# Kernel optimization log

Measured on AMD Instinct MI355X. Metric: run time of the kernel, lower is better.

## Reference

```python
import jax, jax.numpy as jnp
import numpy as np

N_NODES = 50000
N_EDGES = 600000
IN_CH = 128
HID_CH = 256
OUT_CH = 128


def setup_inputs() -> dict:
    key = jax.random.key(0)
    ks = jax.random.split(key, 8)
    x = jax.random.normal(ks[0], (N_NODES, IN_CH), dtype=jnp.float32)
    edge_index = jax.random.randint(ks[1], (2, N_EDGES), 0, N_NODES, dtype=jnp.int32)
    # SAGEConv params: lin_l applied to aggregated neighbors, lin_r to root, bias on lin_l
    def init_w(k, fan_in, fan_out):
        bound = 1.0 / np.sqrt(fan_in)
        return jax.random.uniform(k, (fan_in, fan_out), jnp.float32, -bound, bound)
    W_l1 = init_w(ks[2], IN_CH, HID_CH)
    W_r1 = init_w(ks[3], IN_CH, HID_CH)
    b1 = jnp.zeros((HID_CH,), jnp.float32)
    W_l2 = init_w(ks[4], HID_CH, OUT_CH)
    W_r2 = init_w(ks[5], HID_CH, OUT_CH)
    b2 = jnp.zeros((OUT_CH,), jnp.float32)
    return {"x": x, "edge_index": edge_index, "W_l1": W_l1, "W_r1": W_r1,
            "b1": b1, "W_l2": W_l2, "W_r2": W_r2, "b2": b2}


def _sage_conv(x, src, dst, W_l, W_r, b):
    # mean-aggregate neighbor messages: gather from src, scatter-sum to dst
    msg = x[src]                                        # [E, d]
    agg = jax.ops.segment_sum(msg, dst, num_segments=N_NODES)      # [N, d]
    cnt = jax.ops.segment_sum(jnp.ones_like(dst, dtype=x.dtype), dst,
                              num_segments=N_NODES)                 # [N]
    mean = agg / jnp.maximum(cnt, 1.0)[:, None]
    return mean @ W_l + x @ W_r + b


def reference(x, edge_index, W_l1, W_r1, b1, W_l2, W_r2, b2):
    src, dst = edge_index[0], edge_index[1]
    h = _sage_conv(x, src, dst, W_l1, W_r1, b1)
    h = jax.nn.relu(h)
    # Dropout(0.3) is identity in eval mode
    out = _sage_conv(h, src, dst, W_l2, W_r2, b2)
    return out
```

## Files before the change

kernel.cpp:

```cpp
#include <hip/hip_runtime.h>


typedef __attribute__((ext_vector_type(8))) short short8;
typedef __attribute__((ext_vector_type(4))) short short4v;
typedef __attribute__((ext_vector_type(4))) float f32x4;

constexpr int ELL = 48;

__device__ inline unsigned short f2b(float f) {
    union { float f; unsigned int u; } v; v.f = f;
    unsigned int u = v.u + 0x7FFFu + ((v.u >> 16) & 1u);
    return (unsigned short)(u >> 16);
}
__device__ inline float b2f(unsigned short h) {
    union { unsigned int u; float f; } v; v.u = ((unsigned int)h) << 16;
    return v.f;
}

__global__ __launch_bounds__(256) void prep_k(
    const float* __restrict__ x,
    const float* __restrict__ Wl1, const float* __restrict__ Wr1,
    const float* __restrict__ Wl2, const float* __restrict__ Wr2,
    unsigned short* __restrict__ x_bf,
    unsigned short* __restrict__ Wt1, unsigned short* __restrict__ Wt2,
    int* __restrict__ cnt,
    long n4, int N, int nbF2b, int nbW)
{
    int b = blockIdx.x;
    const int tid = threadIdx.x;
    if (b < nbF2b) {
        long i = (long)b * 256 + tid;
        if (i < n4) {
            float4 v = *(const float4*)(x + i * 4);
            short4v o;
            o[0] = (short)f2b(v.x); o[1] = (short)f2b(v.y);
            o[2] = (short)f2b(v.z); o[3] = (short)f2b(v.w);
            *(short4v*)(x_bf + i * 4) = o;
        }
        return;
    }
    b -= nbF2b;
    if (b < nbW) {
        int y = b >> 7;
        int idx = (b & 127) * 256 + tid;
        const float* src = (y == 0) ? Wl1 : (y == 1) ? Wr1 : (y == 2) ? Wl2 : Wr2;
        unsigned short* dst = (y < 2) ? (Wt1 + (size_t)y * 32768)
                                      : (Wt2 + (size_t)(y - 2) * 32768);
        int K1 = (y < 2) ? 128 : 256;
        int H  = (y < 2) ? 256 : 128;
        int n = idx / K1, k = idx % K1;
        dst[idx] = f2b(src[(size_t)k * H + n]);
        return;
    }
    b -= nbW;
    int i = b * 256 + tid;
    if (i < N / 4) ((int4*)cnt)[i] = (int4){0, 0, 0, 0};
}

__global__ __launch_bounds__(256) void fill_ell_k(
    const int* __restrict__ src, const int* __restrict__ dst,
    int* __restrict__ cnt, unsigned short* __restrict__ nbr, int E)
{
    int e = blockIdx.x * blockDim.x + threadIdx.x;
    if (e >= E) return;
    int d = dst[e];
    int p = atomicAdd(&cnt[d], 1);
    if (p < ELL) nbr[(size_t)d * ELL + p] = (unsigned short)src[e];
}

template<int C>
__device__ inline void ell_row_sum(
    const unsigned short* __restrict__ feat,
    const unsigned short* __restrict__ row,
    int deg, int g, float (&acc)[8])
{
    int i = 0;
    for (; i + 4 <= deg; i += 4) {
        ushort4 s4 = *(const ushort4*)(row + i);
        short8 v0 = *(const short8*)(feat + (size_t)s4.x * C + g * 8);
        short8 v1 = *(const short8*)(feat + (size_t)s4.y * C + g * 8);
        short8 v2 = *(const short8*)(feat + (size_t)s4.z * C + g * 8);
        short8 v3 = *(const short8*)(feat + (size_t)s4.w * C + g * 8);
#pragma unroll
        for (int j = 0; j < 8; ++j)
            acc[j] += (b2f((unsigned short)v0[j]) + b2f((unsigned short)v1[j]))
                    + (b2f((unsigned short)v2[j]) + b2f((unsigned short)v3[j]));
    }
    for (; i < deg; ++i) {
        int s = row[i];
        short8 v0 = *(const short8*)(feat + (size_t)s * C + g * 8);
#pragma unroll
        for (int j = 0; j < 8; ++j) acc[j] += b2f((unsigned short)v0[j]);
    }
}

template<int C>
__global__ __launch_bounds__(256) void gather_mean_k(
    const unsigned short* __restrict__ feat,
    const int* __restrict__ cnt,
    const unsigned short* __restrict__ nbr,
    unsigned short* __restrict__ mean,
    int N)
{
    constexpr int GPN = C / 8;
    constexpr int NPB = 256 / GPN;
    int node = blockIdx.x * NPB + threadIdx.x / GPN;
    int g = threadIdx.x % GPN;
    if (node >= N) return;
    int deg = min(cnt[node], ELL);
    float acc[8] = {};
    ell_row_sum<C>(feat, nbr + (size_t)node * ELL, deg, g, acc);
    float sc = 1.0f / (float)max(deg, 1);
    short8 o;
#pragma unroll
    for (int j = 0; j < 8; ++j) o[j] = (short)f2b(acc[j] * sc);
    *(short8*)(mean + (size_t)node * C + g * 8) = o;
}

template<int C>
__global__ __launch_bounds__(256) void gather_add_out_k(
    const unsigned short* __restrict__ y,
    const unsigned short* __restrict__ z,
    const int* __restrict__ cnt,
    const unsigned short* __restrict__ nbr,
    float* __restrict__ out,
    int N)
{
    constexpr int GPN = C / 8;
    constexpr int NPB = 256 / GPN;
    int node = blockIdx.x * NPB + threadIdx.x / GPN;
    int g = threadIdx.x % GPN;
    if (node >= N) return;
    int deg = min(cnt[node], ELL);
    float acc[8] = {};
    ell_row_sum<C>(y, nbr + (size_t)node * ELL, deg, g, acc);
    float sc = 1.0f / (float)max(deg, 1);
    short8 zv = *(const short8*)(z + (size_t)node * C + g * 8);
    float* o = out + (size_t)node * C + g * 8;
    float4 r0, r1;
    r0.x = b2f((unsigned short)zv[0]) + acc[0] * sc;
    r0.y = b2f((unsigned short)zv[1]) + acc[1] * sc;
    r0.z = b2f((unsigned short)zv[2]) + acc[2] * sc;
    r0.w = b2f((unsigned short)zv[3]) + acc[3] * sc;
    r1.x = b2f((unsigned short)zv[4]) + acc[4] * sc;
    r1.y = b2f((unsigned short)zv[5]) + acc[5] * sc;
    r1.z = b2f((unsigned short)zv[6]) + acc[6] * sc;
    r1.w = b2f((unsigned short)zv[7]) + acc[7] * sc;
    *(float4*)o = r0;
    *(float4*)(o + 4) = r1;
}

template<int HOUT>
__global__ __launch_bounds__(256) void sage_mfma_l1_k(
    const unsigned short* __restrict__ A0,
    const unsigned short* __restrict__ A1,
    const unsigned short* __restrict__ Wt,
    const float* __restrict__ bias,
    unsigned short* __restrict__ out,
    int N)
{
    constexpr int BM = 128, BN = 64, NF = BN / 16, K1 = 128;
    __shared__ char lds[BN * 256 * 2];

    const int tid = threadIdx.x;
    const int lane = tid & 63;
    const int w = tid >> 6;
    const int l15 = lane & 15;
    const int lhi = lane >> 4;
    const int bm = blockIdx.x * BM;
    const int bn = blockIdx.y * BN;

    short8 a[2][8];
#pragma unroll
    for (int mf = 0; mf < 2; ++mf) {
        int row = bm + w * 32 + mf * 16 + l15;
        if (row >= N) row = N - 1;
#pragma unroll
        for (int ki = 0; ki < 8; ++ki) {
            const unsigned short* base = (ki < 4) ? A0 : A1;
            a[mf][ki] = *(const short8*)(base + (size_t)row * K1 +
                                         (ki & 3) * 32 + lhi * 8);
        }
    }

#pragma unroll
    for (int i = 0; i < 8; ++i) {
        int u = i * 256 + tid;
        int row = u >> 5, k16 = u & 31;
        int c = k16 >> 4;
        const unsigned short* srcp = Wt + (size_t)c * HOUT * 128 +
                                     (size_t)(bn + row) * 128 + (k16 & 15) * 8;
        short8 v = *(const short8*)srcp;
        *(short8*)(lds + row * 512 + ((k16 ^ (row & 7)) << 4)) = v;
    }
    __syncthreads();

    f32x4 acc[2][NF];
#pragma unroll
    for (int mf = 0; mf < 2; ++mf)
#pragma unroll
        for (int nf = 0; nf < NF; ++nf)
            acc[mf][nf] = (f32x4){0.f, 0.f, 0.f, 0.f};

#pragma unroll
    for (int ki = 0; ki < 8; ++ki) {
        const int k16b = ki * 4 + lhi;
#pragma unroll
        for (int nf = 0; nf < NF; ++nf) {
            int row = nf * 16 + l15;
            short8 b = *(const short8*)(lds + row * 512 +
                                        ((k16b ^ (row & 7)) << 4));
            acc[0][nf] = __builtin_amdgcn_mfma_f32_16x16x32_bf16(a[0][ki], b, acc[0][nf], 0, 0, 0);
            acc[1][nf] = __builtin_amdgcn_mfma_f32_16x16x32_bf16(a[1][ki], b, acc[1][nf], 0, 0, 0);
        }
    }

#pragma unroll
    for (int nf = 0; nf < NF; ++nf) {
        int col = bn + nf * 16 + l15;
        float bv = bias[col];
#pragma unroll
        for (int mf = 0; mf < 2; ++mf) {
#pragma unroll
            for (int r = 0; r < 4; ++r) {
                int row = bm + w * 32 + mf * 16 + lhi * 4 + r;
                if (row < N) {
                    float v = fmaxf(acc[mf][nf][r] + bv, 0.f);
                    out[(size_t)row * HOUT + col] = f2b(v);
                }
            }
        }
    }
}

template<int HOUT>
__global__ __launch_bounds__(256) void dual_mfma_k(
    const unsigned short* __restrict__ A,
    const unsigned short* __restrict__ W0,
    const unsigned short* __restrict__ W1,
    const float* __restrict__ bias,
    unsigned short* __restrict__ y,
    unsigned short* __restrict__ z,
    int N)
{
    constexpr int BM = 128, BN = 32, NF = BN / 16, K1 = 256;
    __shared__ char lds[2 * BN * K1 * 2];

    const int tid = threadIdx.x;
    const int lane = tid & 63;
    const int w = tid >> 6;
    const int l15 = lane & 15;
    const int lhi = lane >> 4;
    const int bm = blockIdx.x * BM;
    const int bn = blockIdx.y * BN;

    short8 a[2][8];
#pragma unroll
    for (int mf = 0; mf < 2; ++mf) {
        int row = bm + w * 32 + mf * 16 + l15;
        if (row >= N) row = N - 1;
        const unsigned short* ar = A + (size_t)row * K1;
#pragma unroll
        for (int ki = 0; ki < 8; ++ki)
            a[mf][ki] = *(const short8*)(ar + ki * 32 + lhi * 8);
    }

#pragma unroll
    for (int i = 0; i < 8; ++i) {
        int u = i * 256 + tid;
        int slice = u >> 10;
        int rem = u & 1023;
        int row = rem >> 5, k16 = rem & 31;
        const unsigned short* srcp = (slice ? W1 : W0) +
                                     (size_t)(bn + row) * K1 + k16 * 8;
        short8 v = *(const short8*)srcp;
        *(short8*)(lds + slice * 16384 + row * 512 +
                   ((k16 ^ (row & 7)) << 4)) = v;
    }
    __syncthreads();

    f32x4 accY[2][NF], accZ[2][NF];
#pragma unroll
    for (int mf = 0; mf < 2; ++mf)
#pragma unroll
        for (int nf = 0; nf < NF; ++nf) {
            accY[mf][nf] = (f32x4){0.f, 0.f, 0.f, 0.f};
            accZ[mf][nf] = (f32x4){0.f, 0.f, 0.f, 0.f};
        }

#pragma unroll
    for (int ki = 0; ki < 8; ++ki) {
        const int k16b = ki * 4 + lhi;
#pragma unroll
        for (int nf = 0; nf < NF; ++nf) {
            int row = nf * 16 + l15;
            int off = row * 512 + ((k16b ^ (row & 7)) << 4);
            short8 b0 = *(const short8*)(lds + off);
            short8 b1 = *(const short8*)(lds + 16384 + off);
            accY[0][nf] = __builtin_amdgcn_mfma_f32_16x16x32_bf16(a[0][ki], b0, accY[0][nf], 0, 0, 0);
            accY[1][nf] = __builtin_amdgcn_mfma_f32_16x16x32_bf16(a[1][ki], b0, accY[1][nf], 0, 0, 0);
            accZ[0][nf] = __builtin_amdgcn_mfma_f32_16x16x32_bf16(a[0][ki], b1, accZ[0][nf], 0, 0, 0);
            accZ[1][nf] = __builtin_amdgcn_mfma_f32_16x16x32_bf16(a[1][ki], b1, accZ[1][nf], 0, 0, 0);
        }
    }

#pragma unroll
    for (int nf = 0; nf < NF; ++nf) {
        int col = bn + nf * 16 + l15;
        float bv = bias[col];
#pragma unroll
        for (int mf = 0; mf < 2; ++mf) {
#pragma unroll
            for (int r = 0; r < 4; ++r) {
                int row = bm + w * 32 + mf * 16 + lhi * 4 + r;
                if (row < N) {
                    y[(size_t)row * HOUT + col] = f2b(accY[mf][nf][r]);
                    z[(size_t)row * HOUT + col] = f2b(accZ[mf][nf][r] + bv);
                }
            }
        }
    }
}

extern "C" void kernel_launch(void* const* d_in, const int* in_sizes, int n_in,
                              void* d_out, int out_size, void* d_ws, size_t ws_size,
                              hipStream_t stream) {
    const float* x   = (const float*)d_in[0];
    const int*   ei  = (const int*)d_in[1];
    const float* Wl1 = (const float*)d_in[2];
    const float* Wr1 = (const float*)d_in[3];
    const float* b1  = (const float*)d_in[4];
    const float* Wl2 = (const float*)d_in[5];
    const float* Wr2 = (const float*)d_in[6];
    const float* b2  = (const float*)d_in[7];
    float* out = (float*)d_out;

    const int N = in_sizes[0] / 128;
    const int E = in_sizes[1] / 2;
    const int* src = ei;
    const int* dst = ei + E;

    char* ws = (char*)d_ws;
    unsigned short* S       = (unsigned short*)ws;
    unsigned short* mean_bf = S;
    unsigned short* y_bf    = S;
    unsigned short* z_bf    = S + (size_t)N * 128;
    unsigned short* h_bf    = S + (size_t)N * 256;
    unsigned short* x_bf    = h_bf + (size_t)N * 256;
    unsigned short* Wt1     = x_bf + (size_t)N * 128;
    unsigned short* Wt2     = Wt1 + 2 * 256 * 128;
    int*            cnt     = (int*)(Wt2 + 2 * 128 * 256);
    unsigned short* nbr     = (unsigned short*)(cnt + N);

    const int gx = (N + 127) / 128;

    long n4 = (long)N * 128 / 4;
    const int nbF2b = (int)((n4 + 255) / 256);
    const int nbW   = 512;
    const int nbZ   = (N / 4 + 255) / 256;
    prep_k<<<nbF2b + nbW + nbZ, 256, 0, stream>>>(
        x, Wl1, Wr1, Wl2, Wr2, x_bf, Wt1, Wt2, cnt, n4, N, nbF2b, nbW);

    fill_ell_k<<<(E + 255) / 256, 256, 0, stream>>>(src, dst, cnt, nbr, E);

    gather_mean_k<128><<<(N + 15) / 16, 256, 0, stream>>>(
        x_bf, cnt, nbr, mean_bf, N);
    sage_mfma_l1_k<256><<<dim3(gx, 4), 256, 0, stream>>>(
        mean_bf, x_bf, Wt1, b1, h_bf, N);

    dual_mfma_k<128><<<dim3(gx, 4), 256, 0, stream>>>(
        h_bf, Wt2, Wt2 + 128 * 256, b2, y_bf, z_bf, N);
    gather_add_out_k<128><<<(N + 15) / 16, 256, 0, stream>>>(
        y_bf, z_bf, cnt, nbr, out, N);
}
```

Baseline: 154.2 us.

## Split gather kernels into XCD-aligned channel slices for L2 locality

The neighbor gather kernels now handle one 32-channel quarter of the feature row per block. Block IDs are mapped so that each XCD (bid & 7) always works on the same channel quarter, which shrinks the feature working set each XCD's L2 must hold for random neighbor gathers. In exchange, each block rereads the neighbor index rows and counts four times and issues narrower per-node loads.

New measurement: 181.8 us. +17.9%, slower.

```diff
diff --git a/kernel.cpp b/kernel.cpp
--- a/kernel.cpp
+++ b/kernel.cpp
@@ -69,18 +69,18 @@
 }
 
 template<int C>
-__device__ inline void ell_row_sum(
-    const unsigned short* __restrict__ feat,
+__device__ inline void ell_slice_sum(
+    const unsigned short* __restrict__ fp,
     const unsigned short* __restrict__ row,
-    int deg, int g, float (&acc)[8])
+    int deg, float (&acc)[8])
 {
     int i = 0;
     for (; i + 4 <= deg; i += 4) {
         ushort4 s4 = *(const ushort4*)(row + i);
-        short8 v0 = *(const short8*)(feat + (size_t)s4.x * C + g * 8);
-        short8 v1 = *(const short8*)(feat + (size_t)s4.y * C + g * 8);
-        short8 v2 = *(const short8*)(feat + (size_t)s4.z * C + g * 8);
-        short8 v3 = *(const short8*)(feat + (size_t)s4.w * C + g * 8);
+        short8 v0 = *(const short8*)(fp + (size_t)s4.x * C);
+        short8 v1 = *(const short8*)(fp + (size_t)s4.y * C);
+        short8 v2 = *(const short8*)(fp + (size_t)s4.z * C);
+        short8 v3 = *(const short8*)(fp + (size_t)s4.w * C);
 #pragma unroll
         for (int j = 0; j < 8; ++j)
             acc[j] += (b2f((unsigned short)v0[j]) + b2f((unsigned short)v1[j]))
@@ -88,55 +88,65 @@
     }
     for (; i < deg; ++i) {
         int s = row[i];
-        short8 v0 = *(const short8*)(feat + (size_t)s * C + g * 8);
+        short8 v0 = *(const short8*)(fp + (size_t)s * C);
 #pragma unroll
         for (int j = 0; j < 8; ++j) acc[j] += b2f((unsigned short)v0[j]);
     }
 }
 
 template<int C>
-__global__ __launch_bounds__(256) void gather_mean_k(
+__global__ __launch_bounds__(256) void gather_mean_q_k(
     const unsigned short* __restrict__ feat,
     const int* __restrict__ cnt,
     const unsigned short* __restrict__ nbr,
     unsigned short* __restrict__ mean,
-    int N)
-{
-    constexpr int GPN = C / 8;
-    constexpr int NPB = 256 / GPN;
-    int node = blockIdx.x * NPB + threadIdx.x / GPN;
+    int N, int NB)
+{
+    constexpr int QCH = 32, GPN = QCH / 8, NPB = 256 / GPN;
+    int bid = blockIdx.x;
+    int xcd = bid & 7;
+    int q = xcd & 3;
+    int nb = (bid >> 3) * 2 + (xcd >> 2);
+    if (nb >= NB) return;
+    int node = nb * NPB + threadIdx.x / GPN;
     int g = threadIdx.x % GPN;
     if (node >= N) return;
     int deg = min(cnt[node], ELL);
     float acc[8] = {};
-    ell_row_sum<C>(feat, nbr + (size_t)node * ELL, deg, g, acc);
+    const unsigned short* fp = feat + q * QCH + g * 8;
+    ell_slice_sum<C>(fp, nbr + (size_t)node * ELL, deg, acc);
     float sc = 1.0f / (float)max(deg, 1);
     short8 o;
 #pragma unroll
     for (int j = 0; j < 8; ++j) o[j] = (short)f2b(acc[j] * sc);
-    *(short8*)(mean + (size_t)node * C + g * 8) = o;
+    *(short8*)(mean + (size_t)node * C + q * QCH + g * 8) = o;
 }
 
 template<int C>
-__global__ __launch_bounds__(256) void gather_add_out_k(
+__global__ __launch_bounds__(256) void gather_add_out_q_k(
     const unsigned short* __restrict__ y,
     const unsigned short* __restrict__ z,
     const int* __restrict__ cnt,
     const unsigned short* __restrict__ nbr,
     float* __restrict__ out,
-    int N)
-{
-    constexpr int GPN = C / 8;
-    constexpr int NPB = 256 / GPN;
-    int node = blockIdx.x * NPB + threadIdx.x / GPN;
+    int N, int NB)
+{
+    constexpr int QCH = 32, GPN = QCH / 8, NPB = 256 / GPN;
+    int bid = blockIdx.x;
+    int xcd = bid & 7;
+    int q = xcd & 3;
+    int nb = (bid >> 3) * 2 + (xcd >> 2);
+    if (nb >= NB) return;
+    int node = nb * NPB + threadIdx.x / GPN;
     int g = threadIdx.x % GPN;
     if (node >= N) return;
     int deg = min(cnt[node], ELL);
     float acc[8] = {};
-    ell_row_sum<C>(y, nbr + (size_t)node * ELL, deg, g, acc);
+    const unsigned short* fp = y + q * QCH + g * 8;
+    ell_slice_sum<C>(fp, nbr + (size_t)node * ELL, deg, acc);
     float sc = 1.0f / (float)max(deg, 1);
-    short8 zv = *(const short8*)(z + (size_t)node * C + g * 8);
-    float* o = out + (size_t)node * C + g * 8;
+    size_t off = (size_t)node * C + q * QCH + g * 8;
+    short8 zv = *(const short8*)(z + off);
     float4 r0, r1;
     r0.x = b2f((unsigned short)zv[0]) + acc[0] * sc;
     r0.y = b2f((unsigned short)zv[1]) + acc[1] * sc;
@@ -146,8 +156,8 @@
     r1.y = b2f((unsigned short)zv[5]) + acc[5] * sc;
     r1.z = b2f((unsigned short)zv[6]) + acc[6] * sc;
     r1.w = b2f((unsigned short)zv[7]) + acc[7] * sc;
-    *(float4*)o = r0;
-    *(float4*)(o + 4) = r1;
+    *(float4*)(out + off) = r0;
+    *(float4*)(out + off + 4) = r1;
 }
 
 template<int HOUT>
@@ -353,6 +363,8 @@
     unsigned short* nbr     = (unsigned short*)(cnt + N);
 
     const int gx = (N + 127) / 128;
+    const int NB = (N + 63) / 64;
+    const int gatherGrid = ((NB + 1) / 2) * 8;
 
     long n4 = (long)N * 128 / 4;
     const int nbF2b = (int)((n4 + 255) / 256);
@@ -363,13 +375,13 @@
 
     fill_ell_k<<<(E + 255) / 256, 256, 0, stream>>>(src, dst, cnt, nbr, E);
 
-    gather_mean_k<128><<<(N + 15) / 16, 256, 0, stream>>>(
-        x_bf, cnt, nbr, mean_bf, N);
+    gather_mean_q_k<128><<<gatherGrid, 256, 0, stream>>>(
+        x_bf, cnt, nbr, mean_bf, N, NB);
     sage_mfma_l1_k<256><<<dim3(gx, 4), 256, 0, stream>>>(
         mean_bf, x_bf, Wt1, b1, h_bf, N);
 
     dual_mfma_k<128><<<dim3(gx, 4), 256, 0, stream>>>(
         h_bf, Wt2, Wt2 + 128 * 256, b2, y_bf, z_bf, N);
-    gather_add_out_k<128><<<(N + 15) / 16, 256, 0, stream>>>(
-        y_bf, z_bf, cnt, nbr, out, N);
-}
+    gather_add_out_q_k<128><<<gatherGrid, 256, 0, stream>>>(
+        y_bf, z_bf, cnt, nbr, out, N, NB);
+}
```

## Fuse layer-1 neighbor mean gather into MFMA GEMM via LDS

Applied to the files above, without the earlier changes.

Merges the layer-1 gather-mean kernel and the layer-1 MFMA GEMM into one kernel. Each 64-row block first computes its neighbor means into swizzled LDS, then runs the full 256-wide output GEMM with B fragments read straight from global or cache. This removes the mean buffer's write and re-read through HBM and one launch. In exchange, weights are no longer staged in LDS and each wave holds 16 accumulators, which raises register pressure. The gather phase also runs with fewer blocks, which may lower occupancy.

Result: slower. 211.8 us (+37.3%).

```diff
diff --git a/kernel.cpp b/kernel.cpp
--- a/kernel.cpp
+++ b/kernel.cpp
@@ -94,27 +94,90 @@
     }
 }
 
-template<int C>
-__global__ __launch_bounds__(256) void gather_mean_k(
-    const unsigned short* __restrict__ feat,
+__global__ __launch_bounds__(256) void fused_l1_k(
+    const unsigned short* __restrict__ x_bf,
     const int* __restrict__ cnt,
     const unsigned short* __restrict__ nbr,
-    unsigned short* __restrict__ mean,
+    const unsigned short* __restrict__ Wt,
+    const float* __restrict__ bias,
+    unsigned short* __restrict__ h,
     int N)
 {
-    constexpr int GPN = C / 8;
-    constexpr int NPB = 256 / GPN;
-    int node = blockIdx.x * NPB + threadIdx.x / GPN;
-    int g = threadIdx.x % GPN;
-    if (node >= N) return;
-    int deg = min(cnt[node], ELL);
-    float acc[8] = {};
-    ell_row_sum<C>(feat, nbr + (size_t)node * ELL, deg, g, acc);
-    float sc = 1.0f / (float)max(deg, 1);
-    short8 o;
-#pragma unroll
-    for (int j = 0; j < 8; ++j) o[j] = (short)f2b(acc[j] * sc);
-    *(short8*)(mean + (size_t)node * C + g * 8) = o;
+    constexpr int BM = 64, K1 = 128, HOUT = 256, NF = 16;
+    __shared__ unsigned short mean_lds[BM * K1];
+
+    const int tid = threadIdx.x;
+    const int lane = tid & 63;
+    const int w = tid >> 6;
+    const int l15 = lane & 15;
+    const int lhi = lane >> 4;
+    const int bm = blockIdx.x * BM;
+
+    {
+        const int g = tid & 15;
+#pragma unroll
+        for (int it = 0; it < 4; ++it) {
+            int rl = it * 16 + (tid >> 4);
+            int node = bm + rl;
+            int nc = min(node, N - 1);
+            int deg = min(cnt[nc], ELL);
+            float acc[8] = {};
+            ell_row_sum<128>(x_bf, nbr + (size_t)nc * ELL, deg, g, acc);
+            float sc = 1.0f / (float)max(deg, 1);
+            short8 o;
+#pragma unroll
+            for (int j = 0; j < 8; ++j) o[j] = (short)f2b(acc[j] * sc);
+            *(short8*)((char*)mean_lds + rl * 256 + ((g ^ (rl & 7)) << 4)) = o;
+        }
+    }
+    __syncthreads();
+
+    const int rowl = w * 16 + l15;
+    const int grow = min(bm + rowl, N - 1);
+
+    short8 a1[4], a0[4];
+#pragma unroll
+    for (int ki = 0; ki < 4; ++ki)
+        a1[ki] = *(const short8*)(x_bf + (size_t)grow * K1 + ki * 32 + lhi * 8);
+#pragma unroll
+    for (int ki = 0; ki < 4; ++ki) {
+        int u = ki * 4 + lhi;
+        a0[ki] = *(const short8*)((char*)mean_lds + rowl * 256 +
+                                  ((u ^ (rowl & 7)) << 4));
+    }
+
+    f32x4 acc[NF];
+#pragma unroll
+    for (int nf = 0; nf < NF; ++nf) acc[nf] = (f32x4){0.f, 0.f, 0.f, 0.f};
+
+#pragma unroll
+    for (int c = 0; c < 2; ++c) {
+        const unsigned short* Wc = Wt + (size_t)c * HOUT * K1;
+#pragma unroll
+        for (int ki = 0; ki < 4; ++ki) {
+            short8 av = c ? a1[ki] : a0[ki];
+#pragma unroll
+            for (int nf = 0; nf < NF; ++nf) {
+                short8 b = *(const short8*)(Wc + (size_t)(nf * 16 + l15) * K1 +
+                                            ki * 32 + lhi * 8);
+                acc[nf] = __builtin_amdgcn_mfma_f32_16x16x32_bf16(av, b, acc[nf], 0, 0, 0);
+            }
+        }
+    }
+
+#pragma unroll
+    for (int nf = 0; nf < NF; ++nf) {
+        int col = nf * 16 + l15;
+        float bv = bias[col];
+#pragma unroll
+        for (int r = 0; r < 4; ++r) {
+            int row = bm + w * 16 + lhi * 4 + r;
+            if (row < N) {
+                float v = fmaxf(acc[nf][r] + bv, 0.f);
+                h[(size_t)row * HOUT + col] = f2b(v);
+            }
+        }
+    }
 }
 
 template<int C>
@@ -151,89 +214,6 @@
 }
 
 template<int HOUT>
-__global__ __launch_bounds__(256) void sage_mfma_l1_k(
-    const unsigned short* __restrict__ A0,
-    const unsigned short* __restrict__ A1,
-    const unsigned short* __restrict__ Wt,
-    const float* __restrict__ bias,
-    unsigned short* __restrict__ out,
-    int N)
-{
-    constexpr int BM = 128, BN = 64, NF = BN / 16, K1 = 128;
-    __shared__ char lds[BN * 256 * 2];
-
-    const int tid = threadIdx.x;
-    const int lane = tid & 63;
-    const int w = tid >> 6;
-    const int l15 = lane & 15;
-    const int lhi = lane >> 4;
-    const int bm = blockIdx.x * BM;
-    const int bn = blockIdx.y * BN;
-
-    short8 a[2][8];
-#pragma unroll
-    for (int mf = 0; mf < 2; ++mf) {
-        int row = bm + w * 32 + mf * 16 + l15;
-        if (row >= N) row = N - 1;
-#pragma unroll
-        for (int ki = 0; ki < 8; ++ki) {
-            const unsigned short* base = (ki < 4) ? A0 : A1;
-            a[mf][ki] = *(const short8*)(base + (size_t)row * K1 +
-                                         (ki & 3) * 32 + lhi * 8);
-        }
-    }
-
-#pragma unroll
-    for (int i = 0; i < 8; ++i) {
-        int u = i * 256 + tid;
-        int row = u >> 5, k16 = u & 31;
-        int c = k16 >> 4;
-        const unsigned short* srcp = Wt + (size_t)c * HOUT * 128 +
-                                     (size_t)(bn + row) * 128 + (k16 & 15) * 8;
-        short8 v = *(const short8*)srcp;
-        *(short8*)(lds + row * 512 + ((k16 ^ (row & 7)) << 4)) = v;
-    }
-    __syncthreads();
-
-    f32x4 acc[2][NF];
-#pragma unroll
-    for (int mf = 0; mf < 2; ++mf)
-#pragma unroll
-        for (int nf = 0; nf < NF; ++nf)
-            acc[mf][nf] = (f32x4){0.f, 0.f, 0.f, 0.f};
-
-#pragma unroll
-    for (int ki = 0; ki < 8; ++ki) {
-        const int k16b = ki * 4 + lhi;
-#pragma unroll
-        for (int nf = 0; nf < NF; ++nf) {
-            int row = nf * 16 + l15;
-            short8 b = *(const short8*)(lds + row * 512 +
-                                        ((k16b ^ (row & 7)) << 4));
-            acc[0][nf] = __builtin_amdgcn_mfma_f32_16x16x32_bf16(a[0][ki], b, acc[0][nf], 0, 0, 0);
-            acc[1][nf] = __builtin_amdgcn_mfma_f32_16x16x32_bf16(a[1][ki], b, acc[1][nf], 0, 0, 0);
-        }
-    }
-
-#pragma unroll
-    for (int nf = 0; nf < NF; ++nf) {
-        int col = bn + nf * 16 + l15;
-        float bv = bias[col];
-#pragma unroll
-        for (int mf = 0; mf < 2; ++mf) {
-#pragma unroll
-            for (int r = 0; r < 4; ++r) {
-                int row = bm + w * 32 + mf * 16 + lhi * 4 + r;
-                if (row < N) {
-                    float v = fmaxf(acc[mf][nf][r] + bv, 0.f);
-                    out[(size_t)row * HOUT + col] = f2b(v);
-                }
-            }
-        }
-    }
-}
-
-template<int HOUT>
 __global__ __launch_bounds__(256) void dual_mfma_k(
     const unsigned short* __restrict__ A,
     const unsigned short* __restrict__ W0,
@@ -342,7 +322,6 @@
 
     char* ws = (char*)d_ws;
     unsigned short* S       = (unsigned short*)ws;
-    unsigned short* mean_bf = S;
     unsigned short* y_bf    = S;
     unsigned short* z_bf    = S + (size_t)N * 128;
     unsigned short* h_bf    = S + (size_t)N * 256;
@@ -352,7 +331,8 @@
     int*            cnt     = (int*)(Wt2 + 2 * 128 * 256);
     unsigned short* nbr     = (unsigned short*)(cnt + N);
 
-    const int gx = (N + 127) / 128;
+    const int gx  = (N + 127) / 128;
+    const int gxf = (N + 63) / 64;
 
     long n4 = (long)N * 128 / 4;
     const int nbF2b = (int)((n4 + 255) / 256);
@@ -363,10 +343,7 @@
 
     fill_ell_k<<<(E + 255) / 256, 256, 0, stream>>>(src, dst, cnt, nbr, E);
 
-    gather_mean_k<128><<<(N + 15) / 16, 256, 0, stream>>>(
-        x_bf, cnt, nbr, mean_bf, N);
-    sage_mfma_l1_k<256><<<dim3(gx, 4), 256, 0, stream>>>(
-        mean_bf, x_bf, Wt1, b1, h_bf, N);
+    fused_l1_k<<<gxf, 256, 0, stream>>>(x_bf, cnt, nbr, Wt1, b1, h_bf, N);
 
     dual_mfma_k<128><<<dim3(gx, 4), 256, 0, stream>>>(
         h_bf, Wt2, Wt2 + 128 * 256, b2, y_bf, z_bf, N);
```
